# Performance work log

Hardware: AMD Instinct MI355X
Metric: run time of the kernel (lower is better)

The kernel has to match this reference:

```python
import jax, jax.numpy as jnp
import numpy as np

BN_EPS = 1e-6
LN_EPS = 1e-5
ROPE_BASE = 10000.0


def rope(x):
    # x: [..., S, d] ; standard half-split rotary embedding, positions 0..S-1
    S, d = x.shape[-2], x.shape[-1]
    half = d // 2
    inv_freq = 1.0 / (ROPE_BASE ** (jnp.arange(half, dtype=jnp.float32) / half))
    ang = jnp.arange(S, dtype=jnp.float32)[:, None] * inv_freq[None, :]  # [S, half]
    cos, sin = jnp.cos(ang), jnp.sin(ang)
    x1, x2 = x[..., :half], x[..., half:]
    return jnp.concatenate([x1 * cos - x2 * sin, x1 * sin + x2 * cos], axis=-1)


def layernorm(x, g, b):
    m = jnp.mean(x, axis=-1, keepdims=True)
    v = jnp.mean((x - m) ** 2, axis=-1, keepdims=True)
    return (x - m) * jax.lax.rsqrt(v + LN_EPS) * g + b


def rms_batchnorm(x, g, b, running):
    # eval-mode RMSBatchNorm1D: normalize by running RMS^2 buffer
    return x * jax.lax.rsqrt(running + BN_EPS) * g + b


def setup_inputs() -> dict:
    B, S, C, H, QD, KD, VD = 4, 2048, 1536, 8, 128, 128, 192
    key = jax.random.key(0)
    ks = jax.random.split(key, 8)
    sc = 0.02
    return {
        'x': jax.random.normal(ks[0], (B, S, C), dtype=jnp.float32),
        'rms_g': jnp.ones((C,), jnp.float32),
        'rms_b': jnp.zeros((C,), jnp.float32),
        'rms_r': jnp.ones((C,), jnp.float32),
        'Wq': jax.random.normal(ks[1], (H * QD, C), jnp.float32) * sc,
        'Wk': jax.random.normal(ks[2], (KD, C), jnp.float32) * sc,
        'Wv': jax.random.normal(ks[3], (VD, C), jnp.float32) * sc,
        'q_g': jnp.ones((QD,), jnp.float32), 'q_b': jnp.zeros((QD,), jnp.float32),
        'k_g': jnp.ones((KD,), jnp.float32), 'k_b': jnp.zeros((KD,), jnp.float32),
        'v_g': jnp.ones((VD,), jnp.float32), 'v_b': jnp.zeros((VD,), jnp.float32),
        'Wo': jax.random.normal(ks[4], (C, H * VD), jnp.float32) * sc,
        'bo': jnp.zeros((C,), jnp.float32),
        'on_g': jnp.ones((C,), jnp.float32),
        'on_b': jnp.zeros((C,), jnp.float32),
        'on_r': jnp.ones((C,), jnp.float32),
    }


def reference(x, rms_g, rms_b, rms_r, Wq, Wk, Wv, q_g, q_b, k_g, k_b, v_g, v_b, Wo, bo, on_g, on_b, on_r):
    B, S, C = x.shape
    H, QD = 8, Wq.shape[0] // 8
    KD, VD = Wk.shape[0], Wv.shape[0]

    xn = rms_batchnorm(x, rms_g, rms_b, rms_r)

    q = (xn @ Wq.T).reshape(B, S, H, QD)       # [B,S,H,QD]
    q = layernorm(q, q_g, q_b)
    k = layernorm(xn @ Wk.T, k_g, k_b)          # [B,S,KD] shared across heads (MQA)
    v = layernorm(xn @ Wv.T, v_g, v_b)          # [B,S,VD]

    # RoPE along sequence dim
    q = rope(jnp.transpose(q, (0, 2, 1, 3)))    # [B,H,S,QD]
    k = rope(k)
    v = rope(v)

    scale = 1.0 / jnp.sqrt(jnp.float32(KD))
    logits = jnp.einsum('bhsc,bSc->bhsS', q, k) * scale   # [B,H,S,S]
    attn = jax.nn.softmax(logits, axis=-1)
    o = jnp.einsum('bhsS,bSc->bshc', attn, v).reshape(B, S, H * VD)

    y = o @ Wo.T + bo                            # [B,S,C]
    y = rms_batchnorm(y, on_g, on_b, on_r)
    # dropout is identity in eval mode
    return y
```

## Files before the change

kernel.cpp:

```cpp
#include <hip/hip_runtime.h>
#include <math.h>

typedef unsigned short u16;
typedef unsigned int   u32;
typedef __attribute__((ext_vector_type(8))) short bf16x8;
typedef __attribute__((ext_vector_type(4))) float f32x4;

#define DEVI static __device__ __forceinline__

constexpr int Bb = 4, Ss = 2048, Cc = 1536, Hh = 8, QD = 128, KD = 128, VD = 192;
constexpr int NTOK = Bb * Ss;
constexpr int NQKV = Hh*QD + KD + VD;
constexpr int NQKV_PAD = 1536;
constexpr float ATTN_SCALE = 0.08838834764831845f;

constexpr size_t OFF_S1  = 0;
constexpr size_t OFF_B1  = OFF_S1 + Cc*4;
constexpr size_t OFF_S2  = OFF_B1 + Cc*4;
constexpr size_t OFF_B2  = OFF_S2 + Cc*4;
constexpr size_t OFF_CT  = 24576;
constexpr size_t OFF_ST  = OFF_CT  + (size_t)Ss*64*4;
constexpr size_t OFF_CTV = OFF_ST  + (size_t)Ss*64*4;
constexpr size_t OFF_STV = OFF_CTV + (size_t)Ss*96*4;
constexpr size_t OFF_WQKV= OFF_STV + (size_t)Ss*96*4;
constexpr size_t OFF_WO  = OFF_WQKV+ (size_t)NQKV_PAD*Cc*2;
constexpr size_t OFF_XN  = OFF_WO  + (size_t)Cc*Cc*2;
constexpr size_t OFF_QKV = OFF_XN  + (size_t)NTOK*Cc*2;
constexpr size_t OFF_Q   = OFF_QKV + (size_t)NTOK*NQKV*2;
constexpr size_t OFF_K   = OFF_Q   + (size_t)NTOK*(Hh*QD)*2;
constexpr size_t OFF_VT  = OFF_K   + (size_t)NTOK*KD*2;

DEVI u16 f2b(float f) {
  union { float f; u32 u; } v; v.f = f;
  u32 r = v.u + 0x7FFFu + ((v.u >> 16) & 1u);
  return (u16)(r >> 16);
}
DEVI float b2f(u16 h) {
  union { u32 u; float f; } v; v.u = ((u32)h) << 16;
  return v.f;
}
DEVI u32 cvtpk(float lo, float hi) {
  u32 r;
  asm("v_cvt_pk_bf16_f32 %0, %1, %2" : "=v"(r) : "v"(lo), "v"(hi));
  return r;
}
DEVI void gload16(const void* g, void* l) {
  __builtin_amdgcn_global_load_lds(g, l, 16, 0, 0);
}
DEVI f32x4 mfma16(bf16x8 a, bf16x8 b, f32x4 c) {
  return __builtin_amdgcn_mfma_f32_16x16x32_bf16(a, b, c, 0, 0, 0);
}

__global__ __launch_bounds__(256) void k_prep_small(
    const float* __restrict__ rms_g, const float* __restrict__ rms_b, const float* __restrict__ rms_r,
    const float* __restrict__ on_g,  const float* __restrict__ on_b,  const float* __restrict__ on_r,
    const float* __restrict__ bo, char* __restrict__ ws)
{
  int i = blockIdx.x * 256 + threadIdx.x;
  float* s1 = (float*)(ws + OFF_S1);
  float* b1 = (float*)(ws + OFF_B1);
  float* s2 = (float*)(ws + OFF_S2);
  float* b2 = (float*)(ws + OFF_B2);
  float* ct = (float*)(ws + OFF_CT);
  float* st = (float*)(ws + OFF_ST);
  float* ctv= (float*)(ws + OFF_CTV);
  float* stv= (float*)(ws + OFF_STV);
  if (i < Cc) {
    float a = rsqrtf(rms_r[i] + 1e-6f) * rms_g[i];
    s1[i] = a; b1[i] = rms_b[i];
    float c = rsqrtf(on_r[i] + 1e-6f) * on_g[i];
    s2[i] = c; b2[i] = bo[i]*c + on_b[i];
  }
  int j = i - Cc;
  if (j >= 0 && j < Ss*64) {
    int s = j >> 6, f = j & 63;
    float invf = expf(-(float)f * (9.210340371976184f / 64.f));
    float ang = (float)s * invf;
    float sn, cs; sincosf(ang, &sn, &cs);
    ct[j] = cs; st[j] = sn;
  }
  int k = j - Ss*64;
  if (k >= 0 && k < Ss*96) {
    int s = k / 96, f = k - s*96;
    float invf = expf(-(float)f * (9.210340371976184f / 96.f));
    float ang = (float)s * invf;
    float sn, cs; sincosf(ang, &sn, &cs);
    ctv[k] = cs; stv[k] = sn;
  }
}

__global__ __launch_bounds__(256) void k_prep_w(
    const float* __restrict__ Wq, const float* __restrict__ Wk, const float* __restrict__ Wv,
    const float* __restrict__ Wo, char* __restrict__ ws)
{
  u16* wqkv = (u16*)(ws + OFF_WQKV);
  u16* wo   = (u16*)(ws + OFF_WO);
  const int total1 = NQKV_PAD * Cc / 4;
  const int total2 = Cc * Cc / 4;
  for (int i = blockIdx.x*256 + threadIdx.x; i < total1 + total2; i += gridDim.x*256) {
    float4 v = make_float4(0.f, 0.f, 0.f, 0.f);
    u16* dst;
    if (i < total1) {
      int r = i / 384, c = (i - r*384) * 4;
      if (r < 1024)      v = *(const float4*)&Wq[(size_t)r*Cc + c];
      else if (r < 1152) v = *(const float4*)&Wk[(size_t)(r-1024)*Cc + c];
      else if (r < 1344) v = *(const float4*)&Wv[(size_t)(r-1152)*Cc + c];
      dst = wqkv + (size_t)i*4;
    } else {
      int t2 = i - total1;
      v = *(const float4*)&Wo[(size_t)t2*4];
      dst = wo + (size_t)t2*4;
    }
    u32 lo = (u32)f2b(v.x) | ((u32)f2b(v.y) << 16);
    u32 hi = (u32)f2b(v.z) | ((u32)f2b(v.w) << 16);
    *(uint2*)dst = make_uint2(lo, hi);
  }
}

__global__ __launch_bounds__(256) void k_xn(const float* __restrict__ x, char* __restrict__ ws)
{
  const float* s1 = (const float*)(ws + OFF_S1);
  const float* b1 = (const float*)(ws + OFF_B1);
  u16* xn = (u16*)(ws + OFF_XN);
  int idx = blockIdx.x*256 + threadIdx.x;
  float4 xv = ((const float4*)x)[idx];
  int c = (idx % (Cc/4)) * 4;
  u32 lo = (u32)f2b(xv.x*s1[c]   + b1[c])   | ((u32)f2b(xv.y*s1[c+1] + b1[c+1]) << 16);
  u32 hi = (u32)f2b(xv.z*s1[c+2] + b1[c+2]) | ((u32)f2b(xv.w*s1[c+3] + b1[c+3]) << 16);
  ((uint2*)xn)[idx] = make_uint2(lo, hi);
}

template <bool EPI>
__global__ __launch_bounds__(512) void k_gemm256(
    const u16* __restrict__ A, const u16* __restrict__ Bw, void* __restrict__ outp,
    int K_, int N_store, const float* __restrict__ s2, const float* __restrict__ b2)
{
  __shared__ u16 tiles[2][2][256*64];
  constexpr int K = Cc;
  constexpr int NT = K / 64;
  constexpr size_t Kb = (size_t)K * 2;
  const int tid = threadIdx.x;
  const int wid = tid >> 6, l = tid & 63;
  const int lr = l & 15, lh = l >> 4;
  const int wr = wid >> 2, wc = wid & 3;
  const int id  = blockIdx.x + gridDim.x * blockIdx.y;
  const int cpx = (gridDim.x * gridDim.y) >> 3;
  const int sw  = (id & 7) * cpx + (id >> 3);
  const int by  = sw / gridDim.x;
  const int bx  = sw - by * gridDim.x;
  const int m0 = by * 256, n0 = bx * 256;

  const int tid8 = tid >> 3;
  const int csrc = (((tid & 7) ^ (tid8 & 7)) << 4);
  const char* aS = (const char*)A  + (size_t)(m0 + tid8) * Kb + csrc;
  const char* bS = (const char*)Bw + (size_t)(n0 + tid8) * Kb + csrc;
  char* ldsW = (char*)&tiles[0][0][0] + wid*1024;

#define STAGE2(bf, t, c0_) {                                                   \
    gload16(((c0_) < 4 ? aS : bS) + (size_t)((c0_)&3)*64*Kb + (size_t)(t)*128, \
            ldsW + (bf)*65536 + ((c0_) < 4 ? 0 : 32768) + ((c0_)&3)*8192);     \
    gload16((((c0_)+1) < 4 ? aS : bS) + (size_t)(((c0_)+1)&3)*64*Kb + (size_t)(t)*128, \
            ldsW + (bf)*65536 + (((c0_)+1) < 4 ? 0 : 32768) + (((c0_)+1)&3)*8192); }

  const int swz = (lr & 7) << 4;
  int baseA[2], baseB[2];
#pragma unroll
  for (int ks = 0; ks < 2; ks++) {
    baseA[ks] = (((wr*128 + lr) * 128) + ks*64 + lh*16) ^ swz;
    baseB[ks] = (((wc*64  + lr) * 128) + ks*64 + lh*16) ^ swz;
  }

  f32x4 acc[8][4] = {};
  bf16x8 fa[4][2], fb0[2][2], fb1[2][2];

  STAGE2(0, 0, 0); STAGE2(0, 0, 2); STAGE2(0, 0, 4); STAGE2(0, 0, 6);

#pragma unroll 1
  for (int t = 0; t < NT; ++t) {
    const int buf = t & 1, nbuf = buf ^ 1;
    const char* la = (const char*)&tiles[buf][0][0];
    const char* lb = (const char*)&tiles[buf][1][0];
    if (t + 1 < NT) {
      STAGE2(nbuf, t+1, 0);
      asm volatile("s_waitcnt vmcnt(2)" ::: "memory");
    } else {
      asm volatile("s_waitcnt vmcnt(0)" ::: "memory");
    }
    __builtin_amdgcn_s_barrier();
#pragma unroll
    for (int mi = 0; mi < 4; mi++)
#pragma unroll
      for (int ks = 0; ks < 2; ks++)
        fa[mi][ks] = *(const bf16x8*)(la + baseA[ks] + mi*2048);
#pragma unroll
    for (int ni = 0; ni < 2; ni++)
#pragma unroll
      for (int ks = 0; ks < 2; ks++)
        fb0[ni][ks] = *(const bf16x8*)(lb + baseB[ks] + ni*2048);
    __builtin_amdgcn_s_setprio(1);
#pragma unroll
    for (int mi = 0; mi < 4; mi++)
#pragma unroll
      for (int ni = 0; ni < 2; ni++)
#pragma unroll
        for (int ks = 0; ks < 2; ks++)
          acc[mi][ni] = mfma16(fa[mi][ks], fb0[ni][ks], acc[mi][ni]);
    __builtin_amdgcn_s_setprio(0);
    __builtin_amdgcn_s_barrier();
#pragma unroll
    for (int ni = 0; ni < 2; ni++)
#pragma unroll
      for (int ks = 0; ks < 2; ks++)
        fb1[ni][ks] = *(const bf16x8*)(lb + baseB[ks] + (2+ni)*2048);
    if (t + 1 < NT) STAGE2(nbuf, t+1, 2);
    __builtin_amdgcn_s_barrier();
    __builtin_amdgcn_s_setprio(1);
#pragma unroll
    for (int mi = 0; mi < 4; mi++)
#pragma unroll
      for (int ni = 0; ni < 2; ni++)
#pragma unroll
        for (int ks = 0; ks < 2; ks++)
          acc[mi][2+ni] = mfma16(fa[mi][ks], fb1[ni][ks], acc[mi][2+ni]);
    __builtin_amdgcn_s_setprio(0);
    __builtin_amdgcn_s_barrier();
#pragma unroll
    for (int mi = 0; mi < 4; mi++)
#pragma unroll
      for (int ks = 0; ks < 2; ks++)
        fa[mi][ks] = *(const bf16x8*)(la + baseA[ks] + (4+mi)*2048);
    if (t + 1 < NT) STAGE2(nbuf, t+1, 4);
    __builtin_amdgcn_s_barrier();
    __builtin_amdgcn_s_setprio(1);
#pragma unroll
    for (int mi = 0; mi < 4; mi++)
#pragma unroll
      for (int ni = 0; ni < 2; ni++)
#pragma unroll
        for (int ks = 0; ks < 2; ks++)
          acc[4+mi][2+ni] = mfma16(fa[mi][ks], fb1[ni][ks], acc[4+mi][2+ni]);
    __builtin_amdgcn_s_setprio(0);
    __builtin_amdgcn_s_barrier();
    if (t + 1 < NT) STAGE2(nbuf, t+1, 6);
    __builtin_amdgcn_s_barrier();
    __builtin_amdgcn_s_setprio(1);
#pragma unroll
    for (int mi = 0; mi < 4; mi++)
#pragma unroll
      for (int ni = 0; ni < 2; ni++)
#pragma unroll
        for (int ks = 0; ks < 2; ks++)
          acc[4+mi][ni] = mfma16(fa[mi][ks], fb0[ni][ks], acc[4+mi][ni]);
    __builtin_amdgcn_s_setprio(0);
    __builtin_amdgcn_s_barrier();
  }
#undef STAGE2

  const int r0 = m0 + wr*128 + lh*4;
  const int c0 = n0 + wc*64 + lr;
#pragma unroll
  for (int mi = 0; mi < 8; mi++) {
#pragma unroll
    for (int ni = 0; ni < 4; ni++) {
      int col = c0 + ni*16;
      if (col < N_store) {
#pragma unroll
        for (int r = 0; r < 4; r++) {
          size_t o = (size_t)(r0 + mi*16 + r) * N_store + col;
          if (EPI) ((float*)outp)[o] = acc[mi][ni][r] * s2[col] + b2[col];
          else     ((u16*)outp)[o]   = f2b(acc[mi][ni][r]);
        }
      }
    }
  }
}

__global__ __launch_bounds__(256) void k_lnrope_qk(
    char* __restrict__ ws,
    const float* __restrict__ q_g, const float* __restrict__ q_b,
    const float* __restrict__ k_g, const float* __restrict__ k_b)
{
  const u16* qkv = (const u16*)(ws + OFF_QKV);
  u16* qo = (u16*)(ws + OFF_Q);
  u16* ko = (u16*)(ws + OFF_K);
  const float* ct = (const float*)(ws + OFF_CT);
  const float* st = (const float*)(ws + OFF_ST);
  const int w = threadIdx.x >> 6, l = threadIdx.x & 63;
  const int rid = blockIdx.x*4 + w;
  const u16* src; u16* dst; const float* g; const float* bb; float osc; int s;
  if (rid < NTOK*Hh) {
    int t = rid >> 3, h = rid & 7;
    s = t & (Ss-1); int b = t >> 11;
    src = qkv + (size_t)t*NQKV + h*QD;
    dst = qo + ((size_t)(b*Hh + h)*Ss + s)*QD;
    g = q_g; bb = q_b; osc = ATTN_SCALE;
  } else {
    int t = rid - NTOK*Hh;
    s = t & (Ss-1);
    src = qkv + (size_t)t*NQKV + Hh*QD;
    dst = ko + (size_t)t*KD;
    g = k_g; bb = k_b; osc = 1.f;
  }
  u32 pk = *(const u32*)(src + 2*l);
  float x0 = b2f((u16)(pk & 0xFFFFu)), x1 = b2f((u16)(pk >> 16));
  float sm = x0 + x1, sq = x0*x0 + x1*x1;
#pragma unroll
  for (int off = 1; off < 64; off <<= 1) { sm += __shfl_xor(sm, off); sq += __shfl_xor(sq, off); }
  float mean = sm * (1.f/128.f);
  float var  = sq * (1.f/128.f) - mean*mean;
  float rstd = rsqrtf(var + 1e-5f);
  int d0 = 2*l;
  float y0 = (x0 - mean)*rstd*g[d0]   + bb[d0];
  float y1 = (x1 - mean)*rstd*g[d0+1] + bb[d0+1];
  float z0 = __shfl_xor(y0, 32);
  float z1 = __shfl_xor(y1, 32);
  int f0 = 2*(l & 31);
  float c0 = ct[s*64 + f0],     s0 = st[s*64 + f0];
  float c1 = ct[s*64 + f0 + 1], s1 = st[s*64 + f0 + 1];
  float o0, o1;
  if (l < 32) { o0 = y0*c0 - z0*s0; o1 = y1*c1 - z1*s1; }
  else        { o0 = z0*s0 + y0*c0; o1 = z1*s1 + y1*c1; }
  o0 *= osc; o1 *= osc;
  *(u32*)(dst + 2*l) = (u32)f2b(o0) | ((u32)f2b(o1) << 16);
}

__global__ __launch_bounds__(256) void k_lnrope_v(
    char* __restrict__ ws, const float* __restrict__ v_g, const float* __restrict__ v_b)
{
  const u16* qkv = (const u16*)(ws + OFF_QKV);
  u16* vo = (u16*)(ws + OFF_VT);
  const float* ct = (const float*)(ws + OFF_CTV);
  const float* st = (const float*)(ws + OFF_STV);
  __shared__ float buf[4][192];
  const int w = threadIdx.x >> 6, l = threadIdx.x & 63;
  const int t = blockIdx.x*4 + w;
  const int s = t & (Ss-1), b = t >> 11;
  const u16* src = qkv + (size_t)t*NQKV + Hh*QD + KD;
  float xs[3]; float sm = 0.f, sq = 0.f;
#pragma unroll
  for (int i2 = 0; i2 < 3; i2++) {
    float xv = b2f(src[l + 64*i2]);
    xs[i2] = xv; buf[w][l + 64*i2] = xv;
    sm += xv; sq += xv*xv;
  }
  __threadfence_block();
#pragma unroll
  for (int off = 1; off < 64; off <<= 1) { sm += __shfl_xor(sm, off); sq += __shfl_xor(sq, off); }
  float mean = sm * (1.f/192.f);
  float var  = sq * (1.f/192.f) - mean*mean;
  float rstd = rsqrtf(var + 1e-5f);
#pragma unroll
  for (int i2 = 0; i2 < 3; i2++) {
    int e = l + 64*i2;
    float val;
    if (e < 96) {
      float x1 = xs[i2], x2 = buf[w][e+96];
      float x1n = (x1-mean)*rstd*v_g[e]    + v_b[e];
      float x2n = (x2-mean)*rstd*v_g[e+96] + v_b[e+96];
      float cs = ct[s*96 + e], sn = st[s*96 + e];
      val = x1n*cs - x2n*sn;
    } else {
      int f = e - 96;
      float x2 = xs[i2], x1 = buf[w][f];
      float x1n = (x1-mean)*rstd*v_g[f] + v_b[f];
      float x2n = (x2-mean)*rstd*v_g[e] + v_b[e];
      float cs = ct[s*96 + f], sn = st[s*96 + f];
      val = x1n*sn + x2n*cs;
    }
    vo[((size_t)b*VD + e)*Ss + s] = f2b(val);
  }
}

__global__ __launch_bounds__(256, 2) void k_attn(const char* __restrict__ ws, u16* __restrict__ O)
{
  const u16* qs = (const u16*)(ws + OFF_Q);
  const u16* ks = (const u16*)(ws + OFF_K);
  const u16* vt = (const u16*)(ws + OFF_VT);
  __shared__ u16 k_lds[64*128];
  __shared__ u16 v_lds[192*64];
  __shared__ u16 p_lds[4][32][64];
  const int tid = threadIdx.x, w = tid >> 6, l = tid & 63;
  const int lr = l & 15, lh = l >> 4;
  const int bid0 = blockIdx.x;
  const int sw = (bid0 & 7)*64 + (bid0 >> 3);
  const int qt = sw & 15, h = (sw >> 4) & 7, b = sw >> 7;
  const int q0 = qt*128 + w*32;
  bf16x8 aq[2][4];
  const u16* qbase = qs + ((size_t)(b*Hh + h)*Ss + q0 + lr)*QD + lh*8;
#pragma unroll
  for (int h2 = 0; h2 < 2; h2++)
#pragma unroll
    for (int kk = 0; kk < 4; kk++)
      aq[h2][kk] = *(const bf16x8*)(qbase + (size_t)h2*16*QD + kk*32);
  float m[2] = {-INFINITY, -INFINITY}, sume[2] = {0.f, 0.f};
  f32x4 acc[2][12] = {};
  const char* ksrc0 = (const char*)(ks + (size_t)b*Ss*KD);
  const char* vsrc0 = (const char*)(vt + (size_t)b*VD*Ss);
  for (int kv0 = 0; kv0 < Ss; kv0 += 64) {
    {
      const char* ksrc = ksrc0 + (size_t)kv0*KD*2;
#pragma unroll
      for (int r = 0; r < 4; r++) {
        int o = r*4096 + w*1024 + l*16;
        gload16(ksrc + (o ^ (((o>>8)&7)<<4)), (char*)k_lds + r*4096 + w*1024);
      }
#pragma unroll
      for (int r = 0; r < 6; r++) {
        int o = r*4096 + w*1024 + l*16;
        int vd = o >> 7, c = o & 127;
        gload16(vsrc0 + (size_t)vd*(Ss*2) + kv0*2 + (c ^ ((vd&7)<<4)),
                (char*)v_lds + r*4096 + w*1024);
      }
    }
    __syncthreads();
    f32x4 sv[2][4] = {};
#pragma unroll
    for (int nt = 0; nt < 4; nt++) {
#pragma unroll
      for (int kk = 0; kk < 4; kk++) {
        int kb = ((nt*16 + lr) << 8) + kk*64 + lh*16;
        kb ^= (lr & 7) << 4;
        bf16x8 bk = *(const bf16x8*)((const char*)k_lds + kb);
        sv[0][nt] = mfma16(bk, aq[0][kk], sv[0][nt]);
        sv[1][nt] = mfma16(bk, aq[1][kk], sv[1][nt]);
      }
    }
#pragma unroll
    for (int h2 = 0; h2 < 2; h2++) {
      float tmx = -INFINITY;
#pragma unroll
      for (int nt = 0; nt < 4; nt++)
        tmx = fmaxf(tmx, fmaxf(fmaxf(sv[h2][nt][0], sv[h2][nt][1]),
                               fmaxf(sv[h2][nt][2], sv[h2][nt][3])));
      tmx = fmaxf(tmx, __shfl_xor(tmx, 16));
      tmx = fmaxf(tmx, __shfl_xor(tmx, 32));
      if (!__all(tmx - m[h2] <= 8.f)) {
        float mnew = fmaxf(m[h2], tmx);
        float scl = __expf(m[h2] - mnew);
        m[h2] = mnew; sume[h2] *= scl;
#pragma unroll
        for (int n = 0; n < 12; n++) acc[h2][n] *= scl;
      }
      float tsum = 0.f;
#pragma unroll
      for (int nt = 0; nt < 4; nt++) {
#pragma unroll
        for (int r2 = 0; r2 < 4; r2++) {
          float e = __expf(sv[h2][nt][r2] - m[h2]);
          sv[h2][nt][r2] = e; tsum += e;
        }
      }
      tsum += __shfl_xor(tsum, 16);
      tsum += __shfl_xor(tsum, 32);
      sume[h2] += tsum;
      {
        char* pw = (char*)&p_lds[w][h2*16 + lr][0];
#pragma unroll
        for (int nt = 0; nt < 4; nt++) {
          u32 w0 = cvtpk(sv[h2][nt][0], sv[h2][nt][1]);
          u32 w1 = cvtpk(sv[h2][nt][2], sv[h2][nt][3]);
          int pcol = (nt*32 + lh*8) ^ ((lr & 7) << 4);
          *(u32*)(pw + pcol)     = w0;
          *(u32*)(pw + pcol + 4) = w1;
        }
      }
    }
    asm volatile("s_waitcnt lgkmcnt(0)" ::: "memory");
    __builtin_amdgcn_sched_barrier(0);
#pragma unroll
    for (int kk2 = 0; kk2 < 2; kk2++) {
      int rcol = (kk2*64 + lh*16) ^ ((lr & 7) << 4);
      bf16x8 pb0 = *(const bf16x8*)((const char*)&p_lds[w][lr][0]      + rcol);
      bf16x8 pb1 = *(const bf16x8*)((const char*)&p_lds[w][16 + lr][0] + rcol);
#pragma unroll
      for (int n = 0; n < 12; n++) {
        int vb = ((n*16 + lr) << 7) + kk2*64 + lh*16;
        vb ^= (lr & 7) << 4;
        bf16x8 av = *(const bf16x8*)((const char*)v_lds + vb);
        acc[0][n] = mfma16(av, pb0, acc[0][n]);
        acc[1][n] = mfma16(av, pb1, acc[1][n]);
      }
    }
    __syncthreads();
  }
#pragma unroll
  for (int h2 = 0; h2 < 2; h2++) {
    float inv = 1.f / sume[h2];
#pragma unroll
    for (int n = 0; n < 12; n++) {
      u32 w0 = cvtpk(acc[h2][n][0]*inv, acc[h2][n][1]*inv);
      u32 w1 = cvtpk(acc[h2][n][2]*inv, acc[h2][n][3]*inv);
      size_t o = ((size_t)b*Ss + q0 + h2*16 + lr)*Cc + h*VD + n*16 + lh*4;
      *(uint2*)(O + o) = make_uint2(w0, w1);
    }
  }
}

extern "C" void kernel_launch(void* const* d_in, const int* in_sizes, int n_in,
                              void* d_out, int out_size, void* d_ws, size_t ws_size,
                              hipStream_t stream)
{
  const float* x     = (const float*)d_in[0];
  const float* rms_g = (const float*)d_in[1];
  const float* rms_b = (const float*)d_in[2];
  const float* rms_r = (const float*)d_in[3];
  const float* Wq    = (const float*)d_in[4];
  const float* Wk    = (const float*)d_in[5];
  const float* Wv    = (const float*)d_in[6];
  const float* q_g   = (const float*)d_in[7];
  const float* q_b   = (const float*)d_in[8];
  const float* k_g   = (const float*)d_in[9];
  const float* k_b   = (const float*)d_in[10];
  const float* v_g   = (const float*)d_in[11];
  const float* v_b   = (const float*)d_in[12];
  const float* Wo    = (const float*)d_in[13];
  const float* bo    = (const float*)d_in[14];
  const float* on_g  = (const float*)d_in[15];
  const float* on_b  = (const float*)d_in[16];
  const float* on_r  = (const float*)d_in[17];
  char* ws = (char*)d_ws;

  k_prep_small<<<dim3((Cc + Ss*64 + Ss*96) / 256), 256, 0, stream>>>(
      rms_g, rms_b, rms_r, on_g, on_b, on_r, bo, ws);
  k_prep_w<<<dim3(1536), 256, 0, stream>>>(Wq, Wk, Wv, Wo, ws);
  k_xn<<<dim3(NTOK*Cc/4/256), 256, 0, stream>>>(x, ws);
  k_gemm256<false><<<dim3(NQKV_PAD/256, NTOK/256), 512, 0, stream>>>(
      (const u16*)(ws + OFF_XN), (const u16*)(ws + OFF_WQKV), (void*)(ws + OFF_QKV),
      Cc, NQKV, nullptr, nullptr);
  k_lnrope_qk<<<dim3((NTOK*Hh + NTOK)/4), 256, 0, stream>>>(ws, q_g, q_b, k_g, k_b);
  k_lnrope_v<<<dim3(NTOK/4), 256, 0, stream>>>(ws, v_g, v_b);
  k_attn<<<dim3(Bb*Hh*(Ss/128)), 256, 0, stream>>>(ws, (u16*)(ws + OFF_XN));
  k_gemm256<true><<<dim3(Cc/256, NTOK/256), 512, 0, stream>>>(
      (const u16*)(ws + OFF_XN), (const u16*)(ws + OFF_WO), d_out,
      Cc, Cc, (const float*)(ws + OFF_S2), (const float*)(ws + OFF_B2));
}
```

Measured before the change: 357.3 us.

## Double-buffer K/V tiles in attention and use 512-thread blocks with 256 queries

The attention kernel now stages the next 64-key K/V tile into a second LDS buffer while computing on the current one, waiting with vmcnt so loads overlap the MFMA work. Blocks grow to 8 waves covering 256 queries each, which halves the grid to 256 blocks and halves the K/V loads issued per query. LDS use roughly doubles, and with launch bounds (512,1) occupancy per CU may drop. The 256-block grid also maps to about one block per CU, so tail and latency hiding rest on the intra-block pipeline.

Result: no change. 363.2 us (+1.7%).

```diff
diff --git a/kernel.cpp b/kernel.cpp
--- a/kernel.cpp
+++ b/kernel.cpp
@@ -371,20 +371,20 @@
   }
 }
 
-__global__ __launch_bounds__(256, 2) void k_attn(const char* __restrict__ ws, u16* __restrict__ O)
+__global__ __launch_bounds__(512, 1) void k_attn(const char* __restrict__ ws, u16* __restrict__ O)
 {
   const u16* qs = (const u16*)(ws + OFF_Q);
   const u16* ks = (const u16*)(ws + OFF_K);
   const u16* vt = (const u16*)(ws + OFF_VT);
-  __shared__ u16 k_lds[64*128];
-  __shared__ u16 v_lds[192*64];
-  __shared__ u16 p_lds[4][32][64];
-  const int tid = threadIdx.x, w = tid >> 6, l = tid & 63;
+  __shared__ u16 k_lds[2][64*128];
+  __shared__ u16 v_lds[2][192*64];
+  __shared__ u16 p_lds[8][32][64];
+  const int tid = threadIdx.x, w = tid >> 3 >> 3, l = tid & 63;
   const int lr = l & 15, lh = l >> 4;
   const int bid0 = blockIdx.x;
-  const int sw = (bid0 & 7)*64 + (bid0 >> 3);
-  const int qt = sw & 15, h = (sw >> 4) & 7, b = sw >> 7;
-  const int q0 = qt*128 + w*32;
+  const int sw = (bid0 & 7)*32 + (bid0 >> 3);
+  const int qt = sw & 7, h = (sw >> 3) & 7, b = sw >> 6;
+  const int q0 = qt*256 + w*32;
   bf16x8 aq[2][4];
   const u16* qbase = qs + ((size_t)(b*Hh + h)*Ss + q0 + lr)*QD + lh*8;
 #pragma unroll
@@ -396,23 +396,36 @@
   f32x4 acc[2][12] = {};
   const char* ksrc0 = (const char*)(ks + (size_t)b*Ss*KD);
   const char* vsrc0 = (const char*)(vt + (size_t)b*VD*Ss);
-  for (int kv0 = 0; kv0 < Ss; kv0 += 64) {
-    {
-      const char* ksrc = ksrc0 + (size_t)kv0*KD*2;
-#pragma unroll
-      for (int r = 0; r < 4; r++) {
-        int o = r*4096 + w*1024 + l*16;
-        gload16(ksrc + (o ^ (((o>>8)&7)<<4)), (char*)k_lds + r*4096 + w*1024);
-      }
-#pragma unroll
-      for (int r = 0; r < 6; r++) {
-        int o = r*4096 + w*1024 + l*16;
-        int vd = o >> 7, c = o & 127;
-        gload16(vsrc0 + (size_t)vd*(Ss*2) + kv0*2 + (c ^ ((vd&7)<<4)),
-                (char*)v_lds + r*4096 + w*1024);
-      }
-    }
-    __syncthreads();
+
+#define STAGEKV(bf, kv0_) {                                                    \
+    const char* ksrc_ = ksrc0 + (size_t)(kv0_)*KD*2;                           \
+    _Pragma("unroll")                                                          \
+    for (int r_ = 0; r_ < 2; r_++) {                                           \
+      int o_ = r_*8192 + tid*16;                                               \
+      gload16(ksrc_ + (o_ ^ (((o_>>8)&7)<<4)),                                 \
+              (char*)&k_lds[bf][0] + r_*8192 + w*1024);                        \
+    }                                                                          \
+    _Pragma("unroll")                                                          \
+    for (int r_ = 0; r_ < 3; r_++) {                                           \
+      int o_ = r_*8192 + tid*16;                                               \
+      int vd_ = o_ >> 7, c_ = o_ & 127;                                        \
+      gload16(vsrc0 + (size_t)vd_*(Ss*2) + (size_t)(kv0_)*2 + (c_ ^ ((vd_&7)<<4)), \
+              (char*)&v_lds[bf][0] + r_*8192 + w*1024);                        \
+    }                                                                          \
+  }
+
+  STAGEKV(0, 0);
+  for (int it = 0; it < 32; ++it) {
+    const int bf = it & 1;
+    __builtin_amdgcn_s_barrier();
+    if (it < 31) {
+      STAGEKV(bf ^ 1, (it + 1) * 64);
+      asm volatile("s_waitcnt vmcnt(5)" ::: "memory");
+    } else {
+      asm volatile("s_waitcnt vmcnt(0)" ::: "memory");
+    }
+    __builtin_amdgcn_s_barrier();
+    __builtin_amdgcn_sched_barrier(0);
     f32x4 sv[2][4] = {};
 #pragma unroll
     for (int nt = 0; nt < 4; nt++) {
@@ -420,7 +433,7 @@
       for (int kk = 0; kk < 4; kk++) {
         int kb = ((nt*16 + lr) << 8) + kk*64 + lh*16;
         kb ^= (lr & 7) << 4;
-        bf16x8 bk = *(const bf16x8*)((const char*)k_lds + kb);
+        bf16x8 bk = *(const bf16x8*)((const char*)&k_lds[bf][0] + kb);
         sv[0][nt] = mfma16(bk, aq[0][kk], sv[0][nt]);
         sv[1][nt] = mfma16(bk, aq[1][kk], sv[1][nt]);
       }
@@ -476,13 +489,13 @@
       for (int n = 0; n < 12; n++) {
         int vb = ((n*16 + lr) << 7) + kk2*64 + lh*16;
         vb ^= (lr & 7) << 4;
-        bf16x8 av = *(const bf16x8*)((const char*)v_lds + vb);
+        bf16x8 av = *(const bf16x8*)((const char*)&v_lds[bf][0] + vb);
         acc[0][n] = mfma16(av, pb0, acc[0][n]);
         acc[1][n] = mfma16(av, pb1, acc[1][n]);
       }
     }
-    __syncthreads();
-  }
+  }
+#undef STAGEKV
 #pragma unroll
   for (int h2 = 0; h2 < 2; h2++) {
     float inv = 1.f / sume[h2];
@@ -529,7 +542,7 @@
       Cc, NQKV, nullptr, nullptr);
   k_lnrope_qk<<<dim3((NTOK*Hh + NTOK)/4), 256, 0, stream>>>(ws, q_g, q_b, k_g, k_b);
   k_lnrope_v<<<dim3(NTOK/4), 256, 0, stream>>>(ws, v_g, v_b);
-  k_attn<<<dim3(Bb*Hh*(Ss/128)), 256, 0, stream>>>(ws, (u16*)(ws + OFF_XN));
+  k_attn<<<dim3(256), 512, 0, stream>>>(ws, (u16*)(ws + OFF_XN));
   k_gemm256<true><<<dim3(Cc/256, NTOK/256), 512, 0, stream>>>(
       (const u16*)(ws + OFF_XN), (const u16*)(ws + OFF_WO), d_out,
       Cc, Cc, (const float*)(ws + OFF_S2), (const float*)(ws + OFF_B2));
```
